# Kernel tuning notes

Hardware: AMD Instinct MI355X
Metric: run time of the kernel (lower is better)

Reference implementation:

```python
import jax, jax.numpy as jnp
import numpy as np

N_NODES = 100000
N_EDGES = 1600000
F_IN = 128
HID = 128
N_CLS = 40


def _glorot(key, shape):
    fan_in, fan_out = shape[0], shape[1]
    lim = (6.0 / (fan_in + fan_out)) ** 0.5
    return jax.random.uniform(key, shape, jnp.float32, -lim, lim)


def setup_inputs() -> dict:
    key = jax.random.key(0)
    ks = jax.random.split(key, 10)
    x = jax.random.normal(ks[0], (N_NODES, F_IN), jnp.float32)
    edge_index = jax.random.randint(ks[1], (2, N_EDGES), 0, N_NODES, jnp.int64)
    return {
        "x": x,
        "edge_index": edge_index,
        "W1l": _glorot(ks[2], (F_IN, HID)),   # applied to aggregated neighbors
        "W1r": _glorot(ks[3], (F_IN, HID)),   # applied to root features
        "b1": jnp.zeros((HID,), jnp.float32),
        "W2l": _glorot(ks[4], (HID, HID)),
        "W2r": _glorot(ks[5], (HID, HID)),
        "b2": jnp.zeros((HID,), jnp.float32),
        "Wout": _glorot(ks[6], (HID, N_CLS)),
        "bout": jnp.zeros((N_CLS,), jnp.float32),
    }


def _sage_conv(x, src, dst, Wl, Wr, b):
    # mean aggregation of neighbor messages x[src] at dst, then linear combine
    msgs = x[src]                                                   # [E, F] gather
    agg = jax.ops.segment_sum(msgs, dst, num_segments=N_NODES)      # [N, F]
    cnt = jax.ops.segment_sum(jnp.ones((src.shape[0],), x.dtype), dst,
                              num_segments=N_NODES)                 # [N]
    agg = agg / jnp.maximum(cnt, 1.0)[:, None]
    return agg @ Wl + x @ Wr + b


def reference(x, edge_index, W1l, W1r, b1, W2l, W2r, b2, Wout, bout):
    src, dst = edge_index[0], edge_index[1]
    h = jax.nn.relu(_sage_conv(x, src, dst, W1l, W1r, b1))
    # dropout is identity in deterministic (eval) reference
    h = jax.nn.relu(_sage_conv(h, src, dst, W2l, W2r, b2))
    return h @ Wout + bout
```

## Files before the change

### kernel.cpp

```cpp
#include <hip/hip_runtime.h>
#include <hip/hip_bf16.h>

#define N_NODES 100000
#define N_EDGES 1600000
#define FDIM 128
#define NCLS 40
#define NCLS_PAD 48

#define NBINS ((N_NODES + 255) / 256)
#define NBLKB 128
#define CHUNKB (N_EDGES / NBLKB)
#define SCANTOT (NBINS * NBLKB)
#define SCANB_NB ((SCANTOT + 1023) / 1024)

#define LPAD 136

#define PACK1 (FDIM * 256)
#define PACK2 (FDIM * 256)
#define PACK3 (NCLS_PAD * FDIM)
#define PACKTOT (PACK1 + PACK2 + PACK3)
#define PACK_NB ((PACKTOT + 255) / 256)
#define CVT_N4 (N_NODES * FDIM / 4)
#define CVT_NB ((CVT_N4 + 255) / 256)

typedef __attribute__((ext_vector_type(8))) short short8;
typedef __attribute__((ext_vector_type(4))) float f32x4;

__device__ __forceinline__ float bf2f(unsigned short u) {
    union { unsigned int i; float f; } v; v.i = ((unsigned int)u) << 16; return v.f;
}
__device__ __forceinline__ unsigned short f2bf(float f) {
    __hip_bfloat16 h = __float2bfloat16(f);
    return *reinterpret_cast<unsigned short*>(&h);
}

__device__ __forceinline__ void pack_one(const float* Wl, const float* Wr, const float* bin,
                                         unsigned short* Bp, float* bout,
                                         int ncols_out, int ncols_src, int Keach, int idx) {
    int K = (Wr != nullptr) ? 2 * Keach : Keach;
    int col = idx / K, k = idx % K;
    float v = 0.f;
    if (col < ncols_src)
        v = (k < Keach) ? Wl[(size_t)k * ncols_src + col]
                        : Wr[(size_t)(k - Keach) * ncols_src + col];
    Bp[((size_t)(k >> 3) * ncols_out + col) * 8 + (k & 7)] = f2bf(v);
    if (k == 0) bout[col] = (col < ncols_src) ? bin[col] : 0.f;
}

__global__ __launch_bounds__(256) void k_prologue(
        const int* __restrict__ dst, int* __restrict__ bh,
        const float4* __restrict__ x4, ushort4* __restrict__ xb4,
        const float* __restrict__ W1l, const float* __restrict__ W1r,
        const float* __restrict__ b1, unsigned short* __restrict__ Bp1, float* __restrict__ b1p,
        const float* __restrict__ W2l, const float* __restrict__ W2r,
        const float* __restrict__ b2, unsigned short* __restrict__ Bp2, float* __restrict__ b2p,
        const float* __restrict__ Wout, const float* __restrict__ bo,
        unsigned short* __restrict__ Bp3, float* __restrict__ b3p) {
    __shared__ unsigned h[NBINS];
    int b = blockIdx.x;
    if (b < NBLKB) {
        for (int r = threadIdx.x; r < NBINS; r += 256) h[r] = 0u;
        __syncthreads();
        int base = b * CHUNKB;
        int end = base + CHUNKB; if (end > N_EDGES) end = N_EDGES;
        for (int e = base + threadIdx.x; e < end; e += 256)
            atomicAdd(&h[dst[e] >> 8], 1u);
        __syncthreads();
        for (int r = threadIdx.x; r < NBINS; r += 256)
            bh[b * NBINS + r] = (int)h[r];
        return;
    }
    b -= NBLKB;
    if (b < CVT_NB) {
        int i = b * 256 + threadIdx.x;
        if (i < CVT_N4) {
            float4 v = x4[i];
            ushort4 o;
            o.x = f2bf(v.x); o.y = f2bf(v.y); o.z = f2bf(v.z); o.w = f2bf(v.w);
            xb4[i] = o;
        }
        return;
    }
    b -= CVT_NB;
    int idx = b * 256 + threadIdx.x;
    if (idx < PACK1) { pack_one(W1l, W1r, b1, Bp1, b1p, FDIM, FDIM, FDIM, idx); return; }
    idx -= PACK1;
    if (idx < PACK2) { pack_one(W2l, W2r, b2, Bp2, b2p, FDIM, FDIM, FDIM, idx); return; }
    idx -= PACK2;
    if (idx < PACK3) { pack_one(Wout, nullptr, bo, Bp3, b3p, NCLS_PAD, NCLS, FDIM, idx); }
}

__global__ __launch_bounds__(1024) void k_scanB1(const int* __restrict__ bh,
                                                 int* __restrict__ obh,
                                                 unsigned* __restrict__ bsumB) {
    __shared__ unsigned wsums[16];
    int t = threadIdx.x;
    int wave = t >> 6, lane = t & 63;
    int g = blockIdx.x * 1024 + t;
    unsigned v = 0u;
    int r = g >> 7, b = g & (NBLKB - 1);
    if (g < SCANTOT) v = (unsigned)bh[b * NBINS + r];
    unsigned val = v;
#pragma unroll
    for (int d = 1; d < 64; d <<= 1) {
        unsigned n = __shfl_up(val, d, 64);
        if (lane >= d) val += n;
    }
    if (lane == 63) wsums[wave] = val;
    __syncthreads();
    if (t < 16) {
        unsigned wv = wsums[t];
#pragma unroll
        for (int d = 1; d < 16; d <<= 1) {
            unsigned n = __shfl_up(wv, d, 64);
            if (t >= d) wv += n;
        }
        wsums[t] = wv;
    }
    __syncthreads();
    unsigned waveoff = (wave > 0) ? wsums[wave - 1] : 0u;
    if (g < SCANTOT) obh[b * NBINS + r] = (int)(waveoff + val - v);
    if (t == 1023) bsumB[blockIdx.x] = wsums[15];
}

__global__ __launch_bounds__(1024) void k_scanB3(int* __restrict__ obh,
                                                 const unsigned* __restrict__ bsumB,
                                                 int* __restrict__ bucketbase) {
    __shared__ unsigned soff[SCANB_NB];
    int t = threadIdx.x;
    if (t < SCANB_NB) soff[t] = bsumB[t];
    __syncthreads();
    if (t == 0) {
        unsigned run = 0;
        for (int i = 0; i < SCANB_NB; ++i) { unsigned v = soff[i]; soff[i] = run; run += v; }
    }
    __syncthreads();
    int g = blockIdx.x * 1024 + t;
    if (g < SCANTOT) {
        int r = g >> 7, b = g & (NBLKB - 1);
        int val = obh[b * NBINS + r] + (int)soff[blockIdx.x];
        obh[b * NBINS + r] = val;
        if (b == 0) bucketbase[r] = val;
    }
    if (g == 0) bucketbase[NBINS] = N_EDGES;
}

__global__ __launch_bounds__(256) void k_binwriteB(const int* __restrict__ src, const int* __restrict__ dst,
                                                   const int* __restrict__ obh,
                                                   unsigned long long* __restrict__ bpack) {
    __shared__ unsigned pos[NBINS];
    for (int r = threadIdx.x; r < NBINS; r += 256)
        pos[r] = (unsigned)obh[blockIdx.x * NBINS + r];
    __syncthreads();
    int base = blockIdx.x * CHUNKB;
    int end = base + CHUNKB; if (end > N_EDGES) end = N_EDGES;
    for (int e = base + threadIdx.x; e < end; e += 256) {
        int d = dst[e];
        unsigned p = atomicAdd(&pos[d >> 8], 1u);
        bpack[p] = ((unsigned long long)(unsigned)d << 32) | (unsigned)src[e];
    }
}

__global__ __launch_bounds__(256) void k_bucket_csr(const unsigned long long* __restrict__ bpack,
                                                    const int* __restrict__ bucketbase,
                                                    int* __restrict__ rowptr,
                                                    int* __restrict__ esrc) {
    __shared__ unsigned c[256];
    __shared__ unsigned ws[4];
    int b = blockIdx.x;
    int t = threadIdx.x;
    int wave = t >> 6, lane = t & 63;
    int bb = bucketbase[b], be = bucketbase[b + 1];
    c[t] = 0u;
    __syncthreads();
    for (int i = bb + t; i < be; i += 256)
        atomicAdd(&c[(unsigned)(bpack[i] >> 32) & 255u], 1u);
    __syncthreads();
    unsigned own = c[t];
    unsigned val = own;
#pragma unroll
    for (int d = 1; d < 64; d <<= 1) {
        unsigned n = __shfl_up(val, d, 64);
        if (lane >= d) val += n;
    }
    if (lane == 63) ws[wave] = val;
    __syncthreads();
    if (t < 4) {
        unsigned wv = ws[t];
#pragma unroll
        for (int d = 1; d < 4; d <<= 1) {
            unsigned n = __shfl_up(wv, d, 64);
            if (t >= d) wv += n;
        }
        ws[t] = wv;
    }
    __syncthreads();
    unsigned excl = ((wave > 0) ? ws[wave - 1] : 0u) + val - own;
    int node = (b << 8) + t;
    if (node < N_NODES) rowptr[node] = bb + (int)excl;
    if (b == NBINS - 1 && t == 0) rowptr[N_NODES] = N_EDGES;
    __syncthreads();
    c[t] = excl;
    __syncthreads();
    for (int i = bb + t; i < be; i += 256) {
        unsigned long long p = bpack[i];
        unsigned slot = atomicAdd(&c[(unsigned)(p >> 32) & 255u], 1u);
        esrc[bb + (int)slot] = (int)(unsigned)p;
    }
}

__global__ void k_aggregate(const unsigned short* __restrict__ feat,
                            const int* __restrict__ esrc,
                            const int* __restrict__ rowptr,
                            unsigned short* __restrict__ out) {
    int node = blockIdx.x * 4 + (threadIdx.x >> 6);
    if (node >= N_NODES) return;
    int lane = threadIdx.x & 63;
    int sub = lane >> 4;
    int fl = lane & 15;
    int s = rowptr[node], e = rowptr[node + 1];
    float a0[8], a1[8];
#pragma unroll
    for (int q = 0; q < 8; ++q) { a0[q] = 0.f; a1[q] = 0.f; }

    int j = s + sub;
    for (; j + 4 < e; j += 8) {
        int sv0 = esrc[j];
        int sv1 = esrc[j + 4];
        short8 v0 = *(const short8*)(feat + (size_t)sv0 * FDIM + fl * 8);
        short8 v1 = *(const short8*)(feat + (size_t)sv1 * FDIM + fl * 8);
#pragma unroll
        for (int q = 0; q < 8; ++q) {
            a0[q] += bf2f((unsigned short)v0[q]);
            a1[q] += bf2f((unsigned short)v1[q]);
        }
    }
    if (j < e) {
        int sv = esrc[j];
        short8 v = *(const short8*)(feat + (size_t)sv * FDIM + fl * 8);
#pragma unroll
        for (int q = 0; q < 8; ++q) a0[q] += bf2f((unsigned short)v[q]);
    }
#pragma unroll
    for (int q = 0; q < 8; ++q) a0[q] += a1[q];
#pragma unroll
    for (int q = 0; q < 8; ++q) {
        a0[q] += __shfl_xor(a0[q], 16, 64);
        a0[q] += __shfl_xor(a0[q], 32, 64);
    }
    int deg = e - s;
    float inv = 1.0f / (float)(deg > 1 ? deg : 1);
    if (sub == 0) {
        short8 o;
#pragma unroll
        for (int q = 0; q < 8; ++q) o[q] = (short)f2bf(a0[q] * inv);
        *(short8*)(out + (size_t)node * FDIM + fl * 8) = o;
    }
}

__global__ __launch_bounds__(256) void k_gemm_layer(
        const unsigned short* __restrict__ A0, const unsigned short* __restrict__ A1,
        const unsigned short* __restrict__ Bp, const float* __restrict__ bias,
        unsigned short* __restrict__ out) {
    int wave = threadIdx.x >> 6;
    int lane = threadIdx.x & 63;
    int rowblk = blockIdx.x * 64 + wave * 16;
    int lrow = lane & 15;
    int kgrp = lane >> 4;
    int arow = rowblk + lrow; if (arow > N_NODES - 1) arow = N_NODES - 1;

    f32x4 acc[8];
#pragma unroll
    for (int c = 0; c < 8; ++c) acc[c] = (f32x4){0.f, 0.f, 0.f, 0.f};

#pragma unroll
    for (int kb = 0; kb < 8; ++kb) {
        const unsigned short* Asrc = (kb < 4) ? A0 : A1;
        int kk = (kb & 3) * 32 + kgrp * 8;
        short8 a = *(const short8*)(Asrc + (size_t)arow * FDIM + kk);
        int k8 = kb * 4 + kgrp;
        const unsigned short* brow = Bp + ((size_t)k8 * FDIM + lrow) * 8;
#pragma unroll
        for (int c = 0; c < 8; ++c) {
            short8 b = *(const short8*)(brow + c * 16 * 8);
            acc[c] = __builtin_amdgcn_mfma_f32_16x16x32_bf16(a, b, acc[c], 0, 0, 0);
        }
    }

    int orowbase = rowblk + kgrp * 4;
#pragma unroll
    for (int c = 0; c < 8; ++c) {
        int col = c * 16 + lrow;
        float bv = bias[col];
#pragma unroll
        for (int i = 0; i < 4; ++i) {
            int r = orowbase + i;
            if (r < N_NODES) {
                float v = acc[c][i] + bv;
                v = fmaxf(v, 0.f);
                out[(size_t)r * FDIM + col] = f2bf(v);
            }
        }
    }
}

__global__ __launch_bounds__(256) void k_gemm_final(
        const unsigned short* __restrict__ A0, const unsigned short* __restrict__ A1,
        const unsigned short* __restrict__ Bp, const float* __restrict__ bias,
        const unsigned short* __restrict__ Bp3, const float* __restrict__ bias3,
        float* __restrict__ out) {
    __shared__ unsigned short Alds[4][16][LPAD];
    int wave = threadIdx.x >> 6;
    int lane = threadIdx.x & 63;
    int rowblk = blockIdx.x * 64 + wave * 16;
    int lrow = lane & 15;
    int kgrp = lane >> 4;
    int arow = rowblk + lrow; if (arow > N_NODES - 1) arow = N_NODES - 1;

    f32x4 acc2[8];
#pragma unroll
    for (int c = 0; c < 8; ++c) acc2[c] = (f32x4){0.f, 0.f, 0.f, 0.f};

#pragma unroll
    for (int kb = 0; kb < 8; ++kb) {
        const unsigned short* Asrc = (kb < 4) ? A0 : A1;
        int kk = (kb & 3) * 32 + kgrp * 8;
        short8 a = *(const short8*)(Asrc + (size_t)arow * FDIM + kk);
        int k8 = kb * 4 + kgrp;
        const unsigned short* brow = Bp + ((size_t)k8 * FDIM + lrow) * 8;
#pragma unroll
        for (int c = 0; c < 8; ++c) {
            short8 b = *(const short8*)(brow + c * 16 * 8);
            acc2[c] = __builtin_amdgcn_mfma_f32_16x16x32_bf16(a, b, acc2[c], 0, 0, 0);
        }
    }

    int srowbase = kgrp * 4;
#pragma unroll
    for (int c = 0; c < 8; ++c) {
        int col = c * 16 + lrow;
        float bv = bias[col];
#pragma unroll
        for (int i = 0; i < 4; ++i) {
            float v = acc2[c][i] + bv;
            v = fmaxf(v, 0.f);
            Alds[wave][srowbase + i][col] = f2bf(v);
        }
    }

    f32x4 acc3[3];
#pragma unroll
    for (int c = 0; c < 3; ++c) acc3[c] = (f32x4){0.f, 0.f, 0.f, 0.f};

#pragma unroll
    for (int kb = 0; kb < 4; ++kb) {
        short8 a = *(const short8*)(&Alds[wave][lrow][kb * 32 + kgrp * 8]);
        int k8 = kb * 4 + kgrp;
        const unsigned short* brow = Bp3 + ((size_t)k8 * NCLS_PAD + lrow) * 8;
#pragma unroll
        for (int c = 0; c < 3; ++c) {
            short8 b = *(const short8*)(brow + c * 16 * 8);
            acc3[c] = __builtin_amdgcn_mfma_f32_16x16x32_bf16(a, b, acc3[c], 0, 0, 0);
        }
    }

    int orowbase = rowblk + kgrp * 4;
#pragma unroll
    for (int c = 0; c < 3; ++c) {
        int col = c * 16 + lrow;
        if (col < NCLS) {
            float bv = bias3[col];
#pragma unroll
            for (int i = 0; i < 4; ++i) {
                int r = orowbase + i;
                if (r < N_NODES)
                    out[(size_t)r * NCLS + col] = acc3[c][i] + bv;
            }
        }
    }
}

extern "C" void kernel_launch(void* const* d_in, const int* in_sizes, int n_in,
                              void* d_out, int out_size, void* d_ws, size_t ws_size,
                              hipStream_t stream) {
    const float* x    = (const float*)d_in[0];
    const int*   ei   = (const int*)d_in[1];
    const float* W1l  = (const float*)d_in[2];
    const float* W1r  = (const float*)d_in[3];
    const float* b1   = (const float*)d_in[4];
    const float* W2l  = (const float*)d_in[5];
    const float* W2r  = (const float*)d_in[6];
    const float* b2   = (const float*)d_in[7];
    const float* Wout = (const float*)d_in[8];
    const float* bout = (const float*)d_in[9];
    const int* src = ei;
    const int* dst = ei + N_EDGES;

    char* ws = (char*)d_ws;
    size_t off = 0;
    auto alloc = [&](size_t bytes) -> void* {
        void* p = ws + off;
        off += (bytes + 255) & ~(size_t)255;
        return p;
    };
    unsigned short* xb   = (unsigned short*)alloc((size_t)N_NODES * FDIM * 2);
    unsigned short* aggn = (unsigned short*)alloc((size_t)N_NODES * FDIM * 2);
    unsigned short* h1   = (unsigned short*)alloc((size_t)N_NODES * FDIM * 2);
    unsigned short* Bp1  = (unsigned short*)alloc((size_t)FDIM * 256 * 2);
    unsigned short* Bp2  = (unsigned short*)alloc((size_t)FDIM * 256 * 2);
    unsigned short* Bp3  = (unsigned short*)alloc((size_t)NCLS_PAD * FDIM * 2);
    float* b1p = (float*)alloc(FDIM * 4);
    float* b2p = (float*)alloc(FDIM * 4);
    float* b3p = (float*)alloc(NCLS_PAD * 4);
    int* rowptr    = (int*)alloc((size_t)(N_NODES + 1) * 4);
    int* esrc      = (int*)alloc((size_t)N_EDGES * 4);
    int* bh        = (int*)alloc((size_t)NBLKB * NBINS * 4);
    int* obh       = (int*)alloc((size_t)NBLKB * NBINS * 4);
    int* bucketbase= (int*)alloc((size_t)(NBINS + 1) * 4);
    unsigned* bsumB = (unsigned*)alloc((size_t)SCANB_NB * 4);
    unsigned long long* bpack = (unsigned long long*)alloc((size_t)N_EDGES * 8);

    int proGrid = NBLKB + CVT_NB + PACK_NB;
    k_prologue<<<proGrid, 256, 0, stream>>>(
        dst, bh, (const float4*)x, (ushort4*)xb,
        W1l, W1r, b1, Bp1, b1p, W2l, W2r, b2, Bp2, b2p, Wout, bout, Bp3, b3p);

    k_scanB1<<<SCANB_NB, 1024, 0, stream>>>(bh, obh, bsumB);
    k_scanB3<<<SCANB_NB, 1024, 0, stream>>>(obh, bsumB, bucketbase);
    k_binwriteB<<<NBLKB, 256, 0, stream>>>(src, dst, obh, bpack);
    k_bucket_csr<<<NBINS, 256, 0, stream>>>(bpack, bucketbase, rowptr, esrc);

    int aggGrid = (N_NODES + 3) / 4;
    int gemmGrid = (N_NODES + 63) / 64;

    k_aggregate<<<aggGrid, 256, 0, stream>>>(xb, esrc, rowptr, aggn);
    k_gemm_layer<<<gemmGrid, 256, 0, stream>>>(aggn, xb, Bp1, b1p, h1);
    k_aggregate<<<aggGrid, 256, 0, stream>>>(h1, esrc, rowptr, aggn);
    k_gemm_final<<<gemmGrid, 256, 0, stream>>>(aggn, h1, Bp2, b2p, Bp3, b3p, (float*)d_out);
}
```

Baseline: 250.9 us.

## Pack bucket entries into 32 bits, double binning blocks, unroll aggregation by four

Bucket entries now store the low 8 bits of dst alongside a 24-bit src index in one 32-bit word instead of a 64-bit pair, halving the traffic through the intermediate bpack buffer. The binning pass uses 256 blocks instead of 128, with the scan index math updated to match. The aggregate kernel gains a 4-way unrolled loop with four accumulator sets so more gathers are in flight. This relies on node ids fitting in 24 bits and adds register pressure in the aggregate kernel.

```diff
diff --git a/kernel.cpp b/kernel.cpp
--- a/kernel.cpp
+++ b/kernel.cpp
@@ -8,7 +8,7 @@
 #define NCLS_PAD 48
 
 #define NBINS ((N_NODES + 255) / 256)
-#define NBLKB 128
+#define NBLKB 256
 #define CHUNKB (N_EDGES / NBLKB)
 #define SCANTOT (NBINS * NBLKB)
 #define SCANB_NB ((SCANTOT + 1023) / 1024)
@@ -98,7 +98,7 @@
     int wave = t >> 6, lane = t & 63;
     int g = blockIdx.x * 1024 + t;
     unsigned v = 0u;
-    int r = g >> 7, b = g & (NBLKB - 1);
+    int r = g >> 8, b = g & (NBLKB - 1);
     if (g < SCANTOT) v = (unsigned)bh[b * NBINS + r];
     unsigned val = v;
 #pragma unroll
@@ -137,7 +137,7 @@
     __syncthreads();
     int g = blockIdx.x * 1024 + t;
     if (g < SCANTOT) {
-        int r = g >> 7, b = g & (NBLKB - 1);
+        int r = g >> 8, b = g & (NBLKB - 1);
         int val = obh[b * NBINS + r] + (int)soff[blockIdx.x];
         obh[b * NBINS + r] = val;
         if (b == 0) bucketbase[r] = val;
@@ -147,7 +147,7 @@
 
 __global__ __launch_bounds__(256) void k_binwriteB(const int* __restrict__ src, const int* __restrict__ dst,
                                                    const int* __restrict__ obh,
-                                                   unsigned long long* __restrict__ bpack) {
+                                                   unsigned* __restrict__ bpack) {
     __shared__ unsigned pos[NBINS];
     for (int r = threadIdx.x; r < NBINS; r += 256)
         pos[r] = (unsigned)obh[blockIdx.x * NBINS + r];
@@ -157,11 +157,11 @@
     for (int e = base + threadIdx.x; e < end; e += 256) {
         int d = dst[e];
         unsigned p = atomicAdd(&pos[d >> 8], 1u);
-        bpack[p] = ((unsigned long long)(unsigned)d << 32) | (unsigned)src[e];
-    }
-}
-
-__global__ __launch_bounds__(256) void k_bucket_csr(const unsigned long long* __restrict__ bpack,
+        bpack[p] = ((unsigned)(d & 255) << 24) | (unsigned)src[e];
+    }
+}
+
+__global__ __launch_bounds__(256) void k_bucket_csr(const unsigned* __restrict__ bpack,
                                                     const int* __restrict__ bucketbase,
                                                     int* __restrict__ rowptr,
                                                     int* __restrict__ esrc) {
@@ -174,7 +174,7 @@
     c[t] = 0u;
     __syncthreads();
     for (int i = bb + t; i < be; i += 256)
-        atomicAdd(&c[(unsigned)(bpack[i] >> 32) & 255u], 1u);
+        atomicAdd(&c[bpack[i] >> 24], 1u);
     __syncthreads();
     unsigned own = c[t];
     unsigned val = own;
@@ -203,9 +203,9 @@
     c[t] = excl;
     __syncthreads();
     for (int i = bb + t; i < be; i += 256) {
-        unsigned long long p = bpack[i];
-        unsigned slot = atomicAdd(&c[(unsigned)(p >> 32) & 255u], 1u);
-        esrc[bb + (int)slot] = (int)(unsigned)p;
+        unsigned p = bpack[i];
+        unsigned slot = atomicAdd(&c[p >> 24], 1u);
+        esrc[bb + (int)slot] = (int)(p & 0x00FFFFFFu);
     }
 }
 
@@ -219,11 +219,28 @@
     int sub = lane >> 4;
     int fl = lane & 15;
     int s = rowptr[node], e = rowptr[node + 1];
-    float a0[8], a1[8];
-#pragma unroll
-    for (int q = 0; q < 8; ++q) { a0[q] = 0.f; a1[q] = 0.f; }
+    float a0[8], a1[8], a2[8], a3[8];
+#pragma unroll
+    for (int q = 0; q < 8; ++q) { a0[q] = 0.f; a1[q] = 0.f; a2[q] = 0.f; a3[q] = 0.f; }
 
     int j = s + sub;
+    for (; j + 12 < e; j += 16) {
+        int sv0 = esrc[j];
+        int sv1 = esrc[j + 4];
+        int sv2 = esrc[j + 8];
+        int sv3 = esrc[j + 12];
+        short8 v0 = *(const short8*)(feat + (size_t)sv0 * FDIM + fl * 8);
+        short8 v1 = *(const short8*)(feat + (size_t)sv1 * FDIM + fl * 8);
+        short8 v2 = *(const short8*)(feat + (size_t)sv2 * FDIM + fl * 8);
+        short8 v3 = *(const short8*)(feat + (size_t)sv3 * FDIM + fl * 8);
+#pragma unroll
+        for (int q = 0; q < 8; ++q) {
+            a0[q] += bf2f((unsigned short)v0[q]);
+            a1[q] += bf2f((unsigned short)v1[q]);
+            a2[q] += bf2f((unsigned short)v2[q]);
+            a3[q] += bf2f((unsigned short)v3[q]);
+        }
+    }
     for (; j + 4 < e; j += 8) {
         int sv0 = esrc[j];
         int sv1 = esrc[j + 4];
@@ -242,7 +259,7 @@
         for (int q = 0; q < 8; ++q) a0[q] += bf2f((unsigned short)v[q]);
     }
 #pragma unroll
-    for (int q = 0; q < 8; ++q) a0[q] += a1[q];
+    for (int q = 0; q < 8; ++q) a0[q] += (a1[q] + a2[q]) + a3[q];
 #pragma unroll
     for (int q = 0; q < 8; ++q) {
         a0[q] += __shfl_xor(a0[q], 16, 64);
@@ -418,7 +435,7 @@
     int* obh       = (int*)alloc((size_t)NBLKB * NBINS * 4);
     int* bucketbase= (int*)alloc((size_t)(NBINS + 1) * 4);
     unsigned* bsumB = (unsigned*)alloc((size_t)SCANB_NB * 4);
-    unsigned long long* bpack = (unsigned long long*)alloc((size_t)N_EDGES * 8);
+    unsigned* bpack = (unsigned*)alloc((size_t)N_EDGES * 4);
 
     int proGrid = NBLKB + CVT_NB + PACK_NB;
     k_prologue<<<proGrid, 256, 0, stream>>>(
```

Result: faster. 244.2 us (-2.7%).
